# Performance work log

Measured on AMD Instinct MI355X. Metric: run time of the kernel, lower is better.

Reference implementation:

```python
import jax, jax.numpy as jnp
import numpy as np

E_LOCAL = 8          # num_experts // ep_size
HIDDEN = 2048
INTER = 1408
M_TOTAL = 8192       # routed tokens on this rank (balanced: 1024 per expert)
BLOCK_N = 128
BLOCK_K = 128


def _dequant_blocked(w, s, bn=BLOCK_N, bk=BLOCK_K):
    """Per-[bn,bk]-block dequant: w[e,n,k] * s[e, n//bn, k//bk].
    Equivalent to the in-accumulator blockwise scaling in the triton kernel,
    since the scale is constant within each (n-block, k-block) tile."""
    E, N, K = w.shape
    wb = w.reshape(E, N // bn, bn, K // bk, bk)
    return (wb * s[:, :, None, :, None]).reshape(E, N, K)


def setup_inputs() -> dict:
    key = jax.random.key(0)
    k1, k2, k3, k4, k5 = jax.random.split(key, 5)
    hidden_states = jax.random.normal(k1, (M_TOTAL, HIDDEN), dtype=jnp.float32)
    # balanced dispatch: equal token count per local expert (tokens sorted by expert)
    tokens_per_expert = jnp.full((E_LOCAL,), M_TOTAL // E_LOCAL, dtype=jnp.int32)
    # fp8 quantized weight values (simulated as f32) + per-128x128-block scales
    gate_up_weight = jax.random.normal(k2, (E_LOCAL, 2 * INTER, HIDDEN), dtype=jnp.float32)
    gate_up_scale = jax.random.uniform(k3, (E_LOCAL, 2 * INTER // BLOCK_N, HIDDEN // BLOCK_K),
                                       dtype=jnp.float32, minval=0.01, maxval=0.05)
    gate_down_weight = jax.random.normal(k4, (E_LOCAL, HIDDEN, INTER), dtype=jnp.float32)
    gate_down_scale = jax.random.uniform(k5, (E_LOCAL, HIDDEN // BLOCK_N, INTER // BLOCK_K),
                                         dtype=jnp.float32, minval=0.01, maxval=0.05)
    return {
        "hidden_states": hidden_states,
        "tokens_per_expert": tokens_per_expert,
        "gate_up_weight": gate_up_weight,
        "gate_up_scale": gate_up_scale,
        "gate_down_weight": gate_down_weight,
        "gate_down_scale": gate_down_scale,
    }


def reference(hidden_states, tokens_per_expert, gate_up_weight, gate_up_scale,
              gate_down_weight, gate_down_scale):
    E, N1, K = gate_up_weight.shape   # N1 = 2*intermediate
    M = hidden_states.shape[0]
    m_per_e = M // E                  # balanced segments (tokens sorted by expert)
    inter = N1 // 2

    # NOTE on per-token activation quant: the original quantizes `a` per
    # (token, 128-wide k-group) with scale = amax/fp8_max and the kernel
    # multiplies the same scale back in the accumulator; in real arithmetic
    # quant->dequant cancels, so we feed hidden_states directly.

    # ---- grouped GEMM 1 (gate_up), blocked fp8 dequant fused as pre-scale ----
    w1 = _dequant_blocked(gate_up_weight, gate_up_scale)         # [E, 2I, K]
    a = hidden_states.reshape(E, m_per_e, K)                     # segment view
    gateup = jnp.einsum('emk,enk->emn', a, w1)                   # [E, m, 2I]

    # ---- silu_and_mul ----
    gate, up = gateup[..., :inter], gateup[..., inter:]
    down_in = jax.nn.silu(gate) * up                             # [E, m, I]

    # ---- grouped GEMM 2 (down), blocked fp8 dequant ----
    w2 = _dequant_blocked(gate_down_weight, gate_down_scale)     # [E, H, I]
    out = jnp.einsum('emi,ehi->emh', down_in, w2)                # [E, m, H]
    return out.reshape(M, -1)
```

## Files before the change

kernel.cpp:

```cpp
#include <hip/hip_runtime.h>
#include <hip/hip_bf16.h>
#include <cstdint>

#define E_LOCAL 8
#define HIDDEN  2048
#define INTER   1408
#define MPE     1024
#define BK      64
#define LDP     72

typedef __attribute__((ext_vector_type(8))) __bf16 bf16x8;
typedef __attribute__((ext_vector_type(4))) float  f32x4;
typedef __attribute__((ext_vector_type(8))) unsigned short u16x8;

__device__ __forceinline__ unsigned short f2b(float f) {
    unsigned int u = __float_as_uint(f);
    unsigned int r = (u + 0x7fffu + ((u >> 16) & 1u)) >> 16;
    return (unsigned short)r;
}

__device__ __forceinline__ void async16(const unsigned short* g, unsigned short* l) {
    __builtin_amdgcn_global_load_lds(
        (const __attribute__((address_space(1))) unsigned int*)g,
        (__attribute__((address_space(3))) unsigned int*)l, 16, 0, 0);
}

#define CONV_C0 1048576u
#define CONV_C1 2883584u
#define CONV_C2 1441792u
#define CONV_BLOCKS ((CONV_C0 + CONV_C1 + CONV_C2) / 256u)

__global__ __launch_bounds__(256) void convert_all(
        const float* __restrict__ hidden, const float* __restrict__ w1,
        const float* __restrict__ s1, const float* __restrict__ w2,
        const float* __restrict__ s2,
        unsigned short* __restrict__ bh, unsigned short* __restrict__ bw1,
        unsigned short* __restrict__ bw2)
{
    unsigned int g = blockIdx.x * 256u + threadIdx.x;
    const float* src; unsigned short* dst; size_t base; float s;
    if (g < CONV_C0) {
        unsigned int r = g >> 7, c16 = g & 127u;
        base = ((size_t)r << 11) + (size_t)c16 * 16;
        s = 1.0f; src = hidden; dst = bh;
    } else if (g < CONV_C0 + CONV_C1) {
        unsigned int li = g - CONV_C0;
        unsigned int r = li >> 7, c16 = li & 127u;
        unsigned int e = r / 2816u, n = r - e * 2816u;
        base = ((size_t)r << 11) + (size_t)c16 * 16;
        s = s1[(e * 22u + (n >> 7)) * 16u + (c16 >> 3)];
        src = w1; dst = bw1;
    } else {
        unsigned int li = g - CONV_C0 - CONV_C1;
        unsigned int r = li / 88u, c16 = li - r * 88u;
        unsigned int e = r >> 11, h = r & 2047u;
        base = (size_t)r * 1408 + (size_t)c16 * 16;
        s = s2[(e * 16u + (h >> 7)) * 11u + (c16 >> 3)];
        src = w2; dst = bw2;
    }
    float4 v0 = *(const float4*)(src + base);
    float4 v1 = *(const float4*)(src + base + 4);
    float4 v2 = *(const float4*)(src + base + 8);
    float4 v3 = *(const float4*)(src + base + 12);
    u16x8 o0, o1;
    o0[0] = f2b(v0.x * s); o0[1] = f2b(v0.y * s); o0[2] = f2b(v0.z * s); o0[3] = f2b(v0.w * s);
    o0[4] = f2b(v1.x * s); o0[5] = f2b(v1.y * s); o0[6] = f2b(v1.z * s); o0[7] = f2b(v1.w * s);
    o1[0] = f2b(v2.x * s); o1[1] = f2b(v2.y * s); o1[2] = f2b(v2.z * s); o1[3] = f2b(v2.w * s);
    o1[4] = f2b(v3.x * s); o1[5] = f2b(v3.y * s); o1[6] = f2b(v3.z * s); o1[7] = f2b(v3.w * s);
    *(u16x8*)(dst + base)     = o0;
    *(u16x8*)(dst + base + 8) = o1;
}

__global__ __launch_bounds__(256, 2) void gemm1_bf16(
        const unsigned short* __restrict__ bh,
        const unsigned short* __restrict__ bw1,
        unsigned short* __restrict__ down_in)
{
    __shared__ alignas(16) unsigned short sA[2][128 * 32];
    __shared__ alignas(16) unsigned short sG[2][128 * 32];
    __shared__ alignas(16) unsigned short sU[2][128 * 32];

    const int my = blockIdx.x;
    const int nx = blockIdx.y;
    const int e  = blockIdx.z;
    const int t  = threadIdx.x;
    const int lane = t & 63;
    const int wave = t >> 6;
    const int wm   = (wave >> 1) * 64;
    const int wn   = (wave & 1) * 64;
    const int l16  = lane & 15;
    const int quad = lane >> 4;

    const unsigned short* Abase = bh  + ((size_t)e * MPE + (size_t)my * 128) * HIDDEN;
    const unsigned short* Gbase = bw1 + ((size_t)e * (2 * INTER) + (size_t)nx * 128) * HIDDEN;
    const unsigned short* Ubase = Gbase + (size_t)INTER * HIDDEN;

    const int cgo = (((lane & 3) ^ ((lane >> 3) & 3)) * 8);
    const size_t g0 = (size_t)(wave * 32 + (lane >> 2)) * HIDDEN + cgo;
    const int lo0 = wave * 1024 + lane * 8;

    const int cb = ((quad ^ ((l16 >> 1) & 3)) * 8);

    f32x4 accg[4][4], accu[4][4];
    #pragma unroll
    for (int i = 0; i < 4; ++i)
        #pragma unroll
        for (int j = 0; j < 4; ++j) { accg[i][j] = {0,0,0,0}; accu[i][j] = {0,0,0,0}; }

    auto stage = [&](int buf, int kt) {
        const size_t go = g0 + (size_t)kt * 32;
        async16(Abase + go,               &sA[buf][lo0]);
        async16(Abase + go + 16 * HIDDEN, &sA[buf][lo0 + 512]);
        async16(Gbase + go,               &sG[buf][lo0]);
        async16(Gbase + go + 16 * HIDDEN, &sG[buf][lo0 + 512]);
        async16(Ubase + go,               &sU[buf][lo0]);
        async16(Ubase + go + 16 * HIDDEN, &sU[buf][lo0 + 512]);
    };

    stage(0, 0);
    #pragma unroll 2
    for (int kt = 0; kt < HIDDEN / 32; ++kt) {
        const int cur = kt & 1;
        __syncthreads();
        if (kt + 1 < HIDDEN / 32) stage(cur ^ 1, kt + 1);
        bf16x8 af[4], gf[4], uf[4];
        #pragma unroll
        for (int i = 0; i < 4; ++i) {
            af[i] = *(const bf16x8*)&sA[cur][(wm + i * 16 + l16) * 32 + cb];
            gf[i] = *(const bf16x8*)&sG[cur][(wn + i * 16 + l16) * 32 + cb];
            uf[i] = *(const bf16x8*)&sU[cur][(wn + i * 16 + l16) * 32 + cb];
        }
        __builtin_amdgcn_s_setprio(1);
        #pragma unroll
        for (int mi = 0; mi < 4; ++mi)
            #pragma unroll
            for (int ni = 0; ni < 4; ++ni) {
                accg[mi][ni] = __builtin_amdgcn_mfma_f32_16x16x32_bf16(af[mi], gf[ni], accg[mi][ni], 0, 0, 0);
                accu[mi][ni] = __builtin_amdgcn_mfma_f32_16x16x32_bf16(af[mi], uf[ni], accu[mi][ni], 0, 0, 0);
            }
        __builtin_amdgcn_s_setprio(0);
    }

    unsigned short* Obase = down_in + ((size_t)e * MPE + (size_t)my * 128) * INTER + (size_t)nx * 128;
    #pragma unroll
    for (int mi = 0; mi < 4; ++mi)
        #pragma unroll
        for (int ni = 0; ni < 4; ++ni)
            #pragma unroll
            for (int r = 0; r < 4; ++r) {
                float g = accg[mi][ni][r];
                float u = accu[mi][ni][r];
                float d = g / (1.f + __expf(-g)) * u;
                int m = wm + mi * 16 + quad * 4 + r;
                int c = wn + ni * 16 + l16;
                Obase[(size_t)m * INTER + c] = f2b(d);
            }
}

__global__ __launch_bounds__(256, 2) void gemm2_bf16(
        const unsigned short* __restrict__ down_in,
        const unsigned short* __restrict__ bw2,
        float* __restrict__ out)
{
    __shared__ alignas(16) unsigned short sA[2][128 * 32];
    __shared__ alignas(16) unsigned short sW[2][128 * 32];

    const int my = blockIdx.x;
    const int nx = blockIdx.y;
    const int e  = blockIdx.z;
    const int t  = threadIdx.x;
    const int lane = t & 63;
    const int wave = t >> 6;
    const int wm   = (wave >> 1) * 64;
    const int wn   = (wave & 1) * 64;
    const int l16  = lane & 15;
    const int quad = lane >> 4;

    const unsigned short* Abase = down_in + ((size_t)e * MPE + (size_t)my * 128) * INTER;
    const unsigned short* Wbase = bw2 + ((size_t)e * HIDDEN + (size_t)nx * 128) * INTER;

    const int cgo = (((lane & 3) ^ ((lane >> 3) & 3)) * 8);
    const size_t g0 = (size_t)(wave * 32 + (lane >> 2)) * INTER + cgo;
    const int lo0 = wave * 1024 + lane * 8;
    const int cb  = ((quad ^ ((l16 >> 1) & 3)) * 8);

    f32x4 acc[4][4];
    #pragma unroll
    for (int i = 0; i < 4; ++i)
        #pragma unroll
        for (int j = 0; j < 4; ++j) acc[i][j] = {0,0,0,0};

    auto stage = [&](int buf, int kt) {
        const size_t go = g0 + (size_t)kt * 32;
        async16(Abase + go,              &sA[buf][lo0]);
        async16(Abase + go + 16 * INTER, &sA[buf][lo0 + 512]);
        async16(Wbase + go,              &sW[buf][lo0]);
        async16(Wbase + go + 16 * INTER, &sW[buf][lo0 + 512]);
    };

    stage(0, 0);
    #pragma unroll 2
    for (int kt = 0; kt < INTER / 32; ++kt) {
        const int cur = kt & 1;
        __syncthreads();
        if (kt + 1 < INTER / 32) stage(cur ^ 1, kt + 1);
        bf16x8 af[4], wf[4];
        #pragma unroll
        for (int i = 0; i < 4; ++i) {
            af[i] = *(const bf16x8*)&sA[cur][(wm + i * 16 + l16) * 32 + cb];
            wf[i] = *(const bf16x8*)&sW[cur][(wn + i * 16 + l16) * 32 + cb];
        }
        __builtin_amdgcn_s_setprio(1);
        #pragma unroll
        for (int mi = 0; mi < 4; ++mi)
            #pragma unroll
            for (int ni = 0; ni < 4; ++ni)
                acc[mi][ni] = __builtin_amdgcn_mfma_f32_16x16x32_bf16(af[mi], wf[ni], acc[mi][ni], 0, 0, 0);
        __builtin_amdgcn_s_setprio(0);
    }

    float* Obase = out + ((size_t)e * MPE + (size_t)my * 128) * HIDDEN + (size_t)nx * 128;
    #pragma unroll
    for (int mi = 0; mi < 4; ++mi)
        #pragma unroll
        for (int ni = 0; ni < 4; ++ni)
            #pragma unroll
            for (int r = 0; r < 4; ++r) {
                int m = wm + mi * 16 + quad * 4 + r;
                int c = wn + ni * 16 + l16;
                Obase[(size_t)m * HIDDEN + c] = acc[mi][ni][r];
            }
}

__global__ __launch_bounds__(256, 2) void gemm1_f32(
        const float* __restrict__ hidden, const float* __restrict__ w1,
        const float* __restrict__ s1, unsigned short* __restrict__ down_in)
{
    __shared__ unsigned short sA[128 * LDP];
    __shared__ unsigned short sG[128 * LDP];
    __shared__ unsigned short sU[128 * LDP];
    const int nx = blockIdx.x, my = blockIdx.y, e = blockIdx.z;
    const int t = threadIdx.x, lane = t & 63, wave = t >> 6;
    const int wm = (wave >> 1) * 64, wn = (wave & 1) * 64;
    const int l16 = lane & 15, quad = lane >> 4;
    const float* Abase = hidden + ((size_t)e * MPE + (size_t)my * 128) * HIDDEN;
    const float* Gbase = w1 + ((size_t)e * (2 * INTER) + (size_t)nx * 128) * HIDDEN;
    const float* Ubase = w1 + ((size_t)e * (2 * INTER) + INTER + (size_t)nx * 128) * HIDDEN;
    f32x4 accg[4][4], accu[4][4];
    #pragma unroll
    for (int i = 0; i < 4; ++i)
        #pragma unroll
        for (int j = 0; j < 4; ++j) { accg[i][j] = {0,0,0,0}; accu[i][j] = {0,0,0,0}; }
    for (int kt = 0; kt < HIDDEN / BK; ++kt) {
        const int k0 = kt * BK;
        const int kb = k0 >> 7;
        const float sg = s1[(e * 22 + nx) * 16 + kb];
        const float su = s1[(e * 22 + 11 + nx) * 16 + kb];
        __syncthreads();
        #pragma unroll
        for (int i = 0; i < 8; ++i) {
            int idx = i * 256 + t; int r = idx >> 4, c4 = idx & 15;
            float4 v = *(const float4*)(Abase + (size_t)r * HIDDEN + k0 + c4 * 4);
            ushort4 p = { f2b(v.x), f2b(v.y), f2b(v.z), f2b(v.w) };
            *(ushort4*)&sA[r * LDP + c4 * 4] = p;
        }
        #pragma unroll
        for (int i = 0; i < 8; ++i) {
            int idx = i * 256 + t; int r = idx >> 4, c4 = idx & 15;
            float4 v = *(const float4*)(Gbase + (size_t)r * HIDDEN + k0 + c4 * 4);
            ushort4 p = { f2b(v.x * sg), f2b(v.y * sg), f2b(v.z * sg), f2b(v.w * sg) };
            *(ushort4*)&sG[r * LDP + c4 * 4] = p;
        }
        #pragma unroll
        for (int i = 0; i < 8; ++i) {
            int idx = i * 256 + t; int r = idx >> 4, c4 = idx & 15;
            float4 v = *(const float4*)(Ubase + (size_t)r * HIDDEN + k0 + c4 * 4);
            ushort4 p = { f2b(v.x * su), f2b(v.y * su), f2b(v.z * su), f2b(v.w * su) };
            *(ushort4*)&sU[r * LDP + c4 * 4] = p;
        }
        __syncthreads();
        #pragma unroll
        for (int kk = 0; kk < BK; kk += 32) {
            bf16x8 af[4], gf[4], uf[4];
            #pragma unroll
            for (int i = 0; i < 4; ++i) {
                af[i] = *(const bf16x8*)&sA[(wm + i * 16 + l16) * LDP + kk + quad * 8];
                gf[i] = *(const bf16x8*)&sG[(wn + i * 16 + l16) * LDP + kk + quad * 8];
                uf[i] = *(const bf16x8*)&sU[(wn + i * 16 + l16) * LDP + kk + quad * 8];
            }
            #pragma unroll
            for (int mi = 0; mi < 4; ++mi)
                #pragma unroll
                for (int ni = 0; ni < 4; ++ni) {
                    accg[mi][ni] = __builtin_amdgcn_mfma_f32_16x16x32_bf16(af[mi], gf[ni], accg[mi][ni], 0, 0, 0);
                    accu[mi][ni] = __builtin_amdgcn_mfma_f32_16x16x32_bf16(af[mi], uf[ni], accu[mi][ni], 0, 0, 0);
                }
        }
    }
    unsigned short* Obase = down_in + ((size_t)e * MPE + (size_t)my * 128) * INTER + (size_t)nx * 128;
    #pragma unroll
    for (int mi = 0; mi < 4; ++mi)
        #pragma unroll
        for (int ni = 0; ni < 4; ++ni)
            #pragma unroll
            for (int r = 0; r < 4; ++r) {
                float g = accg[mi][ni][r], u = accu[mi][ni][r];
                float d = g / (1.f + __expf(-g)) * u;
                int m = wm + mi * 16 + quad * 4 + r, c = wn + ni * 16 + l16;
                Obase[(size_t)m * INTER + c] = f2b(d);
            }
}

__global__ __launch_bounds__(256, 2) void gemm2_f32(
        const unsigned short* __restrict__ down_in, const float* __restrict__ w2,
        const float* __restrict__ s2, float* __restrict__ out)
{
    __shared__ unsigned short sA[128 * LDP];
    __shared__ unsigned short sW[128 * LDP];
    const int nx = blockIdx.x, my = blockIdx.y, e = blockIdx.z;
    const int t = threadIdx.x, lane = t & 63, wave = t >> 6;
    const int wm = (wave >> 1) * 64, wn = (wave & 1) * 64;
    const int l16 = lane & 15, quad = lane >> 4;
    const unsigned short* Abase = down_in + ((size_t)e * MPE + (size_t)my * 128) * INTER;
    const float* Wbase = w2 + ((size_t)e * HIDDEN + (size_t)nx * 128) * INTER;
    f32x4 acc[4][4];
    #pragma unroll
    for (int i = 0; i < 4; ++i)
        #pragma unroll
        for (int j = 0; j < 4; ++j) acc[i][j] = {0,0,0,0};
    for (int kt = 0; kt < INTER / BK; ++kt) {
        const int k0 = kt * BK;
        const float sc = s2[(e * 16 + nx) * 11 + (k0 >> 7)];
        __syncthreads();
        #pragma unroll
        for (int i = 0; i < 4; ++i) {
            int idx = i * 256 + t; int r = idx >> 3, c8 = idx & 7;
            uint4 v = *(const uint4*)(Abase + (size_t)r * INTER + k0 + c8 * 8);
            *(uint4*)&sA[r * LDP + c8 * 8] = v;
        }
        #pragma unroll
        for (int i = 0; i < 8; ++i) {
            int idx = i * 256 + t; int r = idx >> 4, c4 = idx & 15;
            float4 v = *(const float4*)(Wbase + (size_t)r * INTER + k0 + c4 * 4);
            ushort4 p = { f2b(v.x * sc), f2b(v.y * sc), f2b(v.z * sc), f2b(v.w * sc) };
            *(ushort4*)&sW[r * LDP + c4 * 4] = p;
        }
        __syncthreads();
        #pragma unroll
        for (int kk = 0; kk < BK; kk += 32) {
            bf16x8 af[4], wf[4];
            #pragma unroll
            for (int i = 0; i < 4; ++i) {
                af[i] = *(const bf16x8*)&sA[(wm + i * 16 + l16) * LDP + kk + quad * 8];
                wf[i] = *(const bf16x8*)&sW[(wn + i * 16 + l16) * LDP + kk + quad * 8];
            }
            #pragma unroll
            for (int mi = 0; mi < 4; ++mi)
                #pragma unroll
                for (int ni = 0; ni < 4; ++ni)
                    acc[mi][ni] = __builtin_amdgcn_mfma_f32_16x16x32_bf16(af[mi], wf[ni], acc[mi][ni], 0, 0, 0);
        }
    }
    float* Obase = out + ((size_t)e * MPE + (size_t)my * 128) * HIDDEN + (size_t)nx * 128;
    #pragma unroll
    for (int mi = 0; mi < 4; ++mi)
        #pragma unroll
        for (int ni = 0; ni < 4; ++ni)
            #pragma unroll
            for (int r = 0; r < 4; ++r) {
                int m = wm + mi * 16 + quad * 4 + r, c = wn + ni * 16 + l16;
                Obase[(size_t)m * HIDDEN + c] = acc[mi][ni][r];
            }
}

extern "C" void kernel_launch(void* const* d_in, const int* in_sizes, int n_in,
                              void* d_out, int out_size, void* d_ws, size_t ws_size,
                              hipStream_t stream) {
    const float* hidden = (const float*)d_in[0];
    const float* w1 = (const float*)d_in[2];
    const float* s1 = (const float*)d_in[3];
    const float* w2 = (const float*)d_in[4];
    const float* s2 = (const float*)d_in[5];
    float* out = (float*)d_out;

    const size_t SZ_BH  = (size_t)8192 * HIDDEN * 2;
    const size_t SZ_BW1 = (size_t)E_LOCAL * 2 * INTER * HIDDEN * 2;
    const size_t SZ_BW2 = (size_t)E_LOCAL * HIDDEN * INTER * 2;
    const size_t SZ_DI  = (size_t)E_LOCAL * MPE * INTER * 2;
    const size_t NEED = SZ_BH + SZ_BW1 + SZ_BW2 + SZ_DI;

    dim3 blk(256);
    if (ws_size >= NEED) {
        char* w = (char*)d_ws;
        unsigned short* bh      = (unsigned short*)w;            w += SZ_BH;
        unsigned short* bw1     = (unsigned short*)w;            w += SZ_BW1;
        unsigned short* bw2     = (unsigned short*)w;            w += SZ_BW2;
        unsigned short* down_in = (unsigned short*)w;

        convert_all<<<dim3(CONV_BLOCKS), blk, 0, stream>>>(hidden, w1, s1, w2, s2, bh, bw1, bw2);

        gemm1_bf16<<<dim3(MPE / 128, INTER / 128, E_LOCAL), blk, 0, stream>>>(bh, bw1, down_in);
        gemm2_bf16<<<dim3(MPE / 128, HIDDEN / 128, E_LOCAL), blk, 0, stream>>>(down_in, bw2, out);
    } else {
        unsigned short* down_in = (unsigned short*)d_ws;
        gemm1_f32<<<dim3(INTER / 128, MPE / 128, E_LOCAL), blk, 0, stream>>>(hidden, w1, s1, down_in);
        gemm2_f32<<<dim3(HIDDEN / 128, MPE / 128, E_LOCAL), blk, 0, stream>>>(down_in, w2, s2, out);
    }
}
```

Baseline: 605.3 us.

## Triple-buffer GEMM LDS pipeline and coalesce the conversion kernel into float4 chunks

Both bf16 GEMM kernels move from a double-buffered LDS ring with __syncthreads to a three-stage ring. Each iteration waits with explicit vmcnt counts and a raw s_barrier, and issues the loads for tile kt+2 right after reading the current tile's fragments, so global loads have more time to overlap with the MFMAs. The conversion kernel now has each thread handle four strided float4 chunks instead of one contiguous 16-float chunk, which is meant to give more coalesced memory access. The three-stage ring raises LDS use per block (72KB for gemm1), which may limit occupancy, and the hand-written waitcnt values assume the compiler keeps the async-load counting order.

```diff
diff --git a/kernel.cpp b/kernel.cpp
--- a/kernel.cpp
+++ b/kernel.cpp
@@ -25,10 +25,10 @@
         (__attribute__((address_space(3))) unsigned int*)l, 16, 0, 0);
 }
 
-#define CONV_C0 1048576u
-#define CONV_C1 2883584u
-#define CONV_C2 1441792u
-#define CONV_BLOCKS ((CONV_C0 + CONV_C1 + CONV_C2) / 256u)
+#define C0_4 4194304u
+#define C1_4 11534336u
+#define C2_4 5767168u
+#define CONV_BLOCKS ((C0_4 + C1_4 + C2_4) / 1024u)
 
 __global__ __launch_bounds__(256) void convert_all(
         const float* __restrict__ hidden, const float* __restrict__ w1,
@@ -37,48 +37,43 @@
         unsigned short* __restrict__ bh, unsigned short* __restrict__ bw1,
         unsigned short* __restrict__ bw2)
 {
-    unsigned int g = blockIdx.x * 256u + threadIdx.x;
-    const float* src; unsigned short* dst; size_t base; float s;
-    if (g < CONV_C0) {
-        unsigned int r = g >> 7, c16 = g & 127u;
-        base = ((size_t)r << 11) + (size_t)c16 * 16;
-        s = 1.0f; src = hidden; dst = bh;
-    } else if (g < CONV_C0 + CONV_C1) {
-        unsigned int li = g - CONV_C0;
-        unsigned int r = li >> 7, c16 = li & 127u;
-        unsigned int e = r / 2816u, n = r - e * 2816u;
-        base = ((size_t)r << 11) + (size_t)c16 * 16;
-        s = s1[(e * 22u + (n >> 7)) * 16u + (c16 >> 3)];
-        src = w1; dst = bw1;
-    } else {
-        unsigned int li = g - CONV_C0 - CONV_C1;
-        unsigned int r = li / 88u, c16 = li - r * 88u;
-        unsigned int e = r >> 11, h = r & 2047u;
-        base = (size_t)r * 1408 + (size_t)c16 * 16;
-        s = s2[(e * 16u + (h >> 7)) * 11u + (c16 >> 3)];
-        src = w2; dst = bw2;
-    }
-    float4 v0 = *(const float4*)(src + base);
-    float4 v1 = *(const float4*)(src + base + 4);
-    float4 v2 = *(const float4*)(src + base + 8);
-    float4 v3 = *(const float4*)(src + base + 12);
-    u16x8 o0, o1;
-    o0[0] = f2b(v0.x * s); o0[1] = f2b(v0.y * s); o0[2] = f2b(v0.z * s); o0[3] = f2b(v0.w * s);
-    o0[4] = f2b(v1.x * s); o0[5] = f2b(v1.y * s); o0[6] = f2b(v1.z * s); o0[7] = f2b(v1.w * s);
-    o1[0] = f2b(v2.x * s); o1[1] = f2b(v2.y * s); o1[2] = f2b(v2.z * s); o1[3] = f2b(v2.w * s);
-    o1[4] = f2b(v3.x * s); o1[5] = f2b(v3.y * s); o1[6] = f2b(v3.z * s); o1[7] = f2b(v3.w * s);
-    *(u16x8*)(dst + base)     = o0;
-    *(u16x8*)(dst + base + 8) = o1;
-}
-
+    #pragma unroll
+    for (int j = 0; j < 4; ++j) {
+        unsigned int g = blockIdx.x * 1024u + j * 256u + threadIdx.x;
+        const float* src; unsigned short* dst; size_t base; float s;
+        if (g < C0_4) {
+            base = (size_t)g * 4;
+            s = 1.0f; src = hidden; dst = bh;
+        } else if (g < C0_4 + C1_4) {
+            unsigned int li = g - C0_4;
+            unsigned int r = li >> 9;
+            unsigned int kb = (li & 511u) >> 5;
+            unsigned int e = r / 2816u, n = r - e * 2816u;
+            base = (size_t)li * 4;
+            s = s1[(e * 22u + (n >> 7)) * 16u + kb];
+            src = w1; dst = bw1;
+        } else {
+            unsigned int li = g - C0_4 - C1_4;
+            unsigned int r = li / 352u;
+            unsigned int c4 = li - r * 352u;
+            unsigned int e = r >> 11, h = r & 2047u;
+            base = (size_t)li * 4;
+            s = s2[(e * 16u + (h >> 7)) * 11u + (c4 >> 5)];
+            src = w2; dst = bw2;
+        }
+        float4 v = *(const float4*)(src + base);
+        ushort4 o = { f2b(v.x * s), f2b(v.y * s), f2b(v.z * s), f2b(v.w * s) };
+        *(ushort4*)(dst + base) = o;
+    }
+}
+
+#define NT1 (HIDDEN / 32)
 __global__ __launch_bounds__(256, 2) void gemm1_bf16(
         const unsigned short* __restrict__ bh,
         const unsigned short* __restrict__ bw1,
         unsigned short* __restrict__ down_in)
 {
-    __shared__ alignas(16) unsigned short sA[2][128 * 32];
-    __shared__ alignas(16) unsigned short sG[2][128 * 32];
-    __shared__ alignas(16) unsigned short sU[2][128 * 32];
+    __shared__ alignas(16) unsigned short sS[3][3][128 * 32];
 
     const int my = blockIdx.x;
     const int nx = blockIdx.y;
@@ -109,26 +104,36 @@
 
     auto stage = [&](int buf, int kt) {
         const size_t go = g0 + (size_t)kt * 32;
-        async16(Abase + go,               &sA[buf][lo0]);
-        async16(Abase + go + 16 * HIDDEN, &sA[buf][lo0 + 512]);
-        async16(Gbase + go,               &sG[buf][lo0]);
-        async16(Gbase + go + 16 * HIDDEN, &sG[buf][lo0 + 512]);
-        async16(Ubase + go,               &sU[buf][lo0]);
-        async16(Ubase + go + 16 * HIDDEN, &sU[buf][lo0 + 512]);
+        async16(Abase + go,               &sS[buf][0][lo0]);
+        async16(Abase + go + 16 * HIDDEN, &sS[buf][0][lo0 + 512]);
+        async16(Gbase + go,               &sS[buf][1][lo0]);
+        async16(Gbase + go + 16 * HIDDEN, &sS[buf][1][lo0 + 512]);
+        async16(Ubase + go,               &sS[buf][2][lo0]);
+        async16(Ubase + go + 16 * HIDDEN, &sS[buf][2][lo0 + 512]);
     };
 
     stage(0, 0);
-    #pragma unroll 2
-    for (int kt = 0; kt < HIDDEN / 32; ++kt) {
-        const int cur = kt & 1;
-        __syncthreads();
-        if (kt + 1 < HIDDEN / 32) stage(cur ^ 1, kt + 1);
+    stage(1, 1);
+    int buf = 0;
+    for (int kt = 0; kt < NT1; ++kt) {
+        if (kt == NT1 - 1) { asm volatile("s_waitcnt vmcnt(0)" ::: "memory"); }
+        else               { asm volatile("s_waitcnt vmcnt(6)" ::: "memory"); }
+        __builtin_amdgcn_s_barrier();
+        __builtin_amdgcn_sched_barrier(0);
+
+        const unsigned short* bA = sS[buf][0];
+        const unsigned short* bG = sS[buf][1];
+        const unsigned short* bU = sS[buf][2];
         bf16x8 af[4], gf[4], uf[4];
         #pragma unroll
         for (int i = 0; i < 4; ++i) {
-            af[i] = *(const bf16x8*)&sA[cur][(wm + i * 16 + l16) * 32 + cb];
-            gf[i] = *(const bf16x8*)&sG[cur][(wn + i * 16 + l16) * 32 + cb];
-            uf[i] = *(const bf16x8*)&sU[cur][(wn + i * 16 + l16) * 32 + cb];
+            af[i] = *(const bf16x8*)&bA[(wm + i * 16 + l16) * 32 + cb];
+            gf[i] = *(const bf16x8*)&bG[(wn + i * 16 + l16) * 32 + cb];
+            uf[i] = *(const bf16x8*)&bU[(wn + i * 16 + l16) * 32 + cb];
+        }
+        if (kt < NT1 - 2) {
+            int nb = buf + 2; if (nb >= 3) nb -= 3;
+            stage(nb, kt + 2);
         }
         __builtin_amdgcn_s_setprio(1);
         #pragma unroll
@@ -139,6 +144,7 @@
                 accu[mi][ni] = __builtin_amdgcn_mfma_f32_16x16x32_bf16(af[mi], uf[ni], accu[mi][ni], 0, 0, 0);
             }
         __builtin_amdgcn_s_setprio(0);
+        buf = (buf == 2) ? 0 : buf + 1;
     }
 
     unsigned short* Obase = down_in + ((size_t)e * MPE + (size_t)my * 128) * INTER + (size_t)nx * 128;
@@ -157,13 +163,13 @@
             }
 }
 
+#define NT2 (INTER / 32)
 __global__ __launch_bounds__(256, 2) void gemm2_bf16(
         const unsigned short* __restrict__ down_in,
         const unsigned short* __restrict__ bw2,
         float* __restrict__ out)
 {
-    __shared__ alignas(16) unsigned short sA[2][128 * 32];
-    __shared__ alignas(16) unsigned short sW[2][128 * 32];
+    __shared__ alignas(16) unsigned short sS[3][2][128 * 32];
 
     const int my = blockIdx.x;
     const int nx = blockIdx.y;
@@ -192,23 +198,32 @@
 
     auto stage = [&](int buf, int kt) {
         const size_t go = g0 + (size_t)kt * 32;
-        async16(Abase + go,              &sA[buf][lo0]);
-        async16(Abase + go + 16 * INTER, &sA[buf][lo0 + 512]);
-        async16(Wbase + go,              &sW[buf][lo0]);
-        async16(Wbase + go + 16 * INTER, &sW[buf][lo0 + 512]);
+        async16(Abase + go,              &sS[buf][0][lo0]);
+        async16(Abase + go + 16 * INTER, &sS[buf][0][lo0 + 512]);
+        async16(Wbase + go,              &sS[buf][1][lo0]);
+        async16(Wbase + go + 16 * INTER, &sS[buf][1][lo0 + 512]);
     };
 
     stage(0, 0);
-    #pragma unroll 2
-    for (int kt = 0; kt < INTER / 32; ++kt) {
-        const int cur = kt & 1;
-        __syncthreads();
-        if (kt + 1 < INTER / 32) stage(cur ^ 1, kt + 1);
+    stage(1, 1);
+    int buf = 0;
+    for (int kt = 0; kt < NT2; ++kt) {
+        if (kt == NT2 - 1) { asm volatile("s_waitcnt vmcnt(0)" ::: "memory"); }
+        else               { asm volatile("s_waitcnt vmcnt(4)" ::: "memory"); }
+        __builtin_amdgcn_s_barrier();
+        __builtin_amdgcn_sched_barrier(0);
+
+        const unsigned short* bA = sS[buf][0];
+        const unsigned short* bW = sS[buf][1];
         bf16x8 af[4], wf[4];
         #pragma unroll
         for (int i = 0; i < 4; ++i) {
-            af[i] = *(const bf16x8*)&sA[cur][(wm + i * 16 + l16) * 32 + cb];
-            wf[i] = *(const bf16x8*)&sW[cur][(wn + i * 16 + l16) * 32 + cb];
+            af[i] = *(const bf16x8*)&bA[(wm + i * 16 + l16) * 32 + cb];
+            wf[i] = *(const bf16x8*)&bW[(wn + i * 16 + l16) * 32 + cb];
+        }
+        if (kt < NT2 - 2) {
+            int nb = buf + 2; if (nb >= 3) nb -= 3;
+            stage(nb, kt + 2);
         }
         __builtin_amdgcn_s_setprio(1);
         #pragma unroll
@@ -217,6 +232,7 @@
             for (int ni = 0; ni < 4; ++ni)
                 acc[mi][ni] = __builtin_amdgcn_mfma_f32_16x16x32_bf16(af[mi], wf[ni], acc[mi][ni], 0, 0, 0);
         __builtin_amdgcn_s_setprio(0);
+        buf = (buf == 2) ? 0 : buf + 1;
     }
 
     float* Obase = out + ((size_t)e * MPE + (size_t)my * 128) * HIDDEN + (size_t)nx * 128;
```

After: 576.9 us. -4.7%, faster.
